# Kernel tuning notes

Hardware: AMD Instinct MI355X
Metric: run time of the kernel (lower is better)

## Reference

```python
import jax, jax.numpy as jnp
import numpy as np

SMALL = 1e-16
N = 8192      # num_nodes
D_IN = 512    # input_dim
D_LAT = 128   # latent_dim


def setup_inputs() -> dict:
    key = jax.random.key(0)
    ks = jax.random.split(key, 6)
    z = jax.random.normal(ks[0], (N, D_IN), jnp.float32)
    gamma = jax.random.uniform(ks[1], (N, D_IN), jnp.float32)
    delta = jax.random.uniform(ks[2], (N, D_IN), jnp.float32)
    lim = float(np.sqrt(6.0 / (D_IN + D_LAT)))  # glorot-uniform init
    Wz = jax.random.uniform(ks[3], (D_IN, D_LAT), jnp.float32, -lim, lim)
    Wg = jax.random.uniform(ks[4], (D_IN, D_LAT), jnp.float32, -lim, lim)
    Wd = jax.random.uniform(ks[5], (D_IN, D_LAT), jnp.float32, -lim, lim)
    return {
        "z": z, "gamma": gamma, "delta": delta,
        "Wz": Wz, "Wg": Wg, "Wd": Wd,
        "bias": jnp.float32(1.0),
        "w_gam": jnp.float32(0.5),
        "w_del": jnp.float32(0.5),
    }


def reference(z, gamma, delta, Wz, Wg, Wd, bias, w_gam, w_del):
    # column-stochastic transforms (softmax over input_dim axis, as in __init__)
    Tz = jax.nn.softmax(Wz, axis=0)
    Tg = jax.nn.softmax(Wg, axis=0)
    Td = jax.nn.softmax(Wd, axis=0)

    zd = z @ Tz                 # [N, D_LAT]
    gd_raw = gamma @ Tg         # [N, D_LAT]
    dd_raw = delta @ Td         # [N, D_LAT]
    gd = gd_raw + SMALL
    dd = dd_raw + SMALL

    z2 = zd * zd
    # dist_gam[i,j] = sum_k (zd[i,k]-zd[j,k])^2 / gd[i,k]  (sender-scaled)
    # expanded: sum_k z2_i/g_i  +  (1/g_i) . z2_j  -  2 (z_i/g_i) . z_j
    a = jnp.sum(z2 / gd, axis=1)                                  # [N]
    dist_gam = a[:, None] + (1.0 / gd) @ z2.T - 2.0 * (zd / gd) @ zd.T  # [N,N]

    # dist_del[i,j] = sum_k (zd[i,k]-zd[j,k])^2 / dd[j,k]  (receiver-scaled)
    b = jnp.sum(z2 / dd, axis=1)                                  # [N]
    dist_del = z2 @ (1.0 / dd).T - 2.0 * zd @ (zd / dd).T + b[None, :]  # [N,N]

    n = jnp.float32(N)
    x = bias - w_gam * (n * dist_gam) - w_del * (n * dist_del)
    out = jax.nn.sigmoid(x.reshape(-1))                           # [N*N]
    return out, zd, gd_raw, dd_raw
```

## Files before the change

### kernel.cpp

```cpp
#include <hip/hip_runtime.h>
#include <hip/hip_bf16.h>
#include <math.h>


#define NSZ 8192
#define DLAT 128

typedef _Float16 half8 __attribute__((ext_vector_type(8)));
typedef float f32x4 __attribute__((ext_vector_type(4)));

__device__ __forceinline__ void gl_lds16(const void* g, void* l) {
    __builtin_amdgcn_global_load_lds(
        (const __attribute__((address_space(1))) void*)g,
        (__attribute__((address_space(3))) void*)l, 16, 0, 0);
}

__device__ __forceinline__ float fast_sigmoid(float x) {
    float e = __builtin_amdgcn_exp2f(-1.44269504f * x);
    return __builtin_amdgcn_rcpf(1.0f + e);
}

__global__ void softmax_cols(const float* __restrict__ Wz, const float* __restrict__ Wg,
                             const float* __restrict__ Wd, float* __restrict__ T) {
    int col = blockIdx.x & 127;
    int m = blockIdx.x >> 7;
    const float* W = (m == 0) ? Wz : (m == 1 ? Wg : Wd);
    float* To = T + (size_t)m * 65536;
    int l = threadIdx.x;
    float v[8];
    float mx = -3.4e38f;
    for (int i = 0; i < 8; ++i) {
        v[i] = W[(size_t)(i * 64 + l) * 128 + col];
        mx = fmaxf(mx, v[i]);
    }
    for (int off = 32; off; off >>= 1) mx = fmaxf(mx, __shfl_xor(mx, off));
    float s = 0.f;
    for (int i = 0; i < 8; ++i) { v[i] = expf(v[i] - mx); s += v[i]; }
    for (int off = 32; off; off >>= 1) s += __shfl_xor(s, off);
    float inv = 1.0f / s;
    for (int i = 0; i < 8; ++i) To[(size_t)(i * 64 + l) * 128 + col] = v[i] * inv;
}

__global__ __launch_bounds__(128) void gemm3(const float* __restrict__ z,
                                             const float* __restrict__ gamma,
                                             const float* __restrict__ delta,
                                             const float* __restrict__ T,
                                             float* __restrict__ outTail) {
    int m = blockIdx.y;
    const float* A = (m == 0) ? z : (m == 1 ? gamma : delta);
    const float* B = T + (size_t)m * 65536;
    float* C = outTail + (size_t)m * (NSZ * DLAT);
    int rowBase = blockIdx.x * 32;
    __shared__ float As[32 * 34];
    int t = threadIdx.x;
    int tc = t & 15, tr = t >> 4;
    float acc[4][8] = {};
    for (int kt = 0; kt < 16; ++kt) {
        int k0 = kt * 32;
        for (int i = 0; i < 2; ++i) {
            int id = i * 128 + t;
            int r = id >> 3, kk = (id & 7) * 4;
            float4 va = *(const float4*)(A + (size_t)(rowBase + r) * 512 + k0 + kk);
            As[(kk + 0) * 34 + r] = va.x; As[(kk + 1) * 34 + r] = va.y;
            As[(kk + 2) * 34 + r] = va.z; As[(kk + 3) * 34 + r] = va.w;
        }
        __syncthreads();
        for (int kk = 0; kk < 32; ++kk) {
            float a0[4], b0[8];
            *(float4*)a0 = *(const float4*)(&As[kk * 34 + tr * 4]);
            const float* Brow = B + (size_t)(k0 + kk) * 128;
            *(float4*)b0 = *(const float4*)(Brow + tc * 4);
            *(float4*)(b0 + 4) = *(const float4*)(Brow + 64 + tc * 4);
            for (int r = 0; r < 4; ++r)
                for (int c = 0; c < 8; ++c) acc[r][c] = fmaf(a0[r], b0[c], acc[r][c]);
        }
        __syncthreads();
    }
    for (int r = 0; r < 4; ++r) {
        int row = rowBase + tr * 4 + r;
        *(float4*)(C + (size_t)row * 128 + tc * 4) = *(float4*)(&acc[r][0]);
        *(float4*)(C + (size_t)row * 128 + 64 + tc * 4) = *(float4*)(&acc[r][4]);
    }
}

__global__ void build_stacks(const float* __restrict__ zd, const float* __restrict__ gdr,
                             const float* __restrict__ ddr, _Float16* __restrict__ Afp,
                             _Float16* __restrict__ Bfp, float* __restrict__ cvec,
                             float* __restrict__ bco, const float* __restrict__ pb,
                             const float* __restrict__ pwg, const float* __restrict__ pwd) {
    int i = blockIdx.x;
    int k = threadIdx.x;
    float zv = zd[(size_t)i * 128 + k];
    float g = gdr[(size_t)i * 128 + k] + 1e-16f;
    float d = ddr[(size_t)i * 128 + k] + 1e-16f;
    float z2 = zv * zv;
    float u = 1.0f / g, p = 1.0f / d;
    float v = zv * u, q = zv * p;
    float wg = *pwg, wd = *pwd, bias = *pb;
    _Float16* Ar = Afp + (size_t)i * 512;
    _Float16* Br = Bfp + (size_t)i * 512;
    Ar[k]       = (_Float16)(wg * u);
    Ar[128 + k] = (_Float16)(wg * v);
    Ar[256 + k] = (_Float16)(wd * z2);
    Ar[384 + k] = (_Float16)(wd * zv);
    Br[k]       = (_Float16)(z2);
    Br[128 + k] = (_Float16)(-2.0f * zv);
    Br[256 + k] = (_Float16)(p);
    Br[384 + k] = (_Float16)(-2.0f * q);
    float a = z2 * u, b = z2 * p;
    for (int off = 32; off; off >>= 1) { a += __shfl_down(a, off); b += __shfl_down(b, off); }
    __shared__ float sa[2], sb[2];
    if ((k & 63) == 0) { sa[k >> 6] = a; sb[k >> 6] = b; }
    __syncthreads();
    if (k == 0) {
        cvec[i] = bias - 8192.0f * wg * (sa[0] + sa[1]);
        bco[i] = 8192.0f * wd * (sb[0] + sb[1]);
    }
}

__global__ __launch_bounds__(256) void pair_kernel(const _Float16* __restrict__ Afp,
                                                   const _Float16* __restrict__ Bfp,
                                                   const float* __restrict__ cvec,
                                                   const float* __restrict__ bco,
                                                   const float* __restrict__ pbias,
                                                   float* __restrict__ out) {
    int bid = blockIdx.x;
    int super = bid >> 6, within = bid & 63;
    int sy = super >> 3, sx = super & 7;
    int by = sy * 8 + (within >> 3), bx = sx * 8 + (within & 7);
    int iBase = by * 128, jBase = bx * 128;

    __shared__ _Float16 As[128 * 64];
    __shared__ _Float16 Bs[128 * 64];
    int t = threadIdx.x;
    int l = t & 63, w = t >> 6;
    int wm = (w >> 1) * 64, wn = (w & 1) * 64;
    int lc = l & 15, lq = l >> 4;
    f32x4 acc[4][4] = {};

    int srow = l >> 3;
    int sq = (l & 7) ^ srow;

    for (int kt = 0; kt < 8; ++kt) {
        int k0 = kt * 64;
        for (int s = 0; s < 4; ++s) {
            int rr = (w * 4 + s) * 8 + srow;
            const _Float16* ga = Afp + (size_t)(iBase + rr) * 512 + k0 + sq * 8;
            const _Float16* gb = Bfp + (size_t)(jBase + rr) * 512 + k0 + sq * 8;
            gl_lds16(ga, &As[(w * 4 + s) * 512]);
            gl_lds16(gb, &Bs[(w * 4 + s) * 512]);
        }
        __syncthreads();
        for (int ks = 0; ks < 2; ++ks) {
            half8 af[4], bf[4];
            for (int mi = 0; mi < 4; ++mi) {
                int r = wm + mi * 16 + lc;
                int q = ks * 4 + lq;
                af[mi] = *(const half8*)(&As[((r << 3) + (q ^ (r & 7))) << 3]);
            }
            for (int ni = 0; ni < 4; ++ni) {
                int r = wn + ni * 16 + lc;
                int q = ks * 4 + lq;
                bf[ni] = *(const half8*)(&Bs[((r << 3) + (q ^ (r & 7))) << 3]);
            }
            for (int mi = 0; mi < 4; ++mi)
                for (int ni = 0; ni < 4; ++ni)
                    acc[mi][ni] = __builtin_amdgcn_mfma_f32_16x16x32_f16(af[mi], bf[ni],
                                                                         acc[mi][ni], 0, 0, 0);
        }
        __syncthreads();
    }

    float bias = *pbias;
    float civ[4][4], bjv[4];
    for (int mi = 0; mi < 4; ++mi)
        for (int r = 0; r < 4; ++r)
            civ[mi][r] = cvec[iBase + wm + mi * 16 + lq * 4 + r];
    for (int ni = 0; ni < 4; ++ni) bjv[ni] = bco[jBase + wn + ni * 16 + lc];

    for (int mi = 0; mi < 4; ++mi) {
        for (int ni = 0; ni < 4; ++ni) {
            for (int r = 0; r < 4; ++r) {
                int i = iBase + wm + mi * 16 + lq * 4 + r;
                int j = jBase + wn + ni * 16 + lc;
                float x = civ[mi][r] - bjv[ni] - 8192.0f * acc[mi][ni][r];
                if (i == j) x = bias;
                out[(size_t)i * NSZ + j] = fast_sigmoid(x);
            }
        }
    }
}

extern "C" void kernel_launch(void* const* d_in, const int* in_sizes, int n_in,
                              void* d_out, int out_size, void* d_ws, size_t ws_size,
                              hipStream_t stream) {
    const float* z = (const float*)d_in[0];
    const float* gamma = (const float*)d_in[1];
    const float* delta = (const float*)d_in[2];
    const float* Wz = (const float*)d_in[3];
    const float* Wg = (const float*)d_in[4];
    const float* Wd = (const float*)d_in[5];
    const float* pb = (const float*)d_in[6];
    const float* pwg = (const float*)d_in[7];
    const float* pwd = (const float*)d_in[8];

    float* out = (float*)d_out;
    float* zd_out = out + (size_t)NSZ * NSZ;
    float* gd_out = zd_out + (size_t)NSZ * DLAT;
    float* dd_out = gd_out + (size_t)NSZ * DLAT;

    float* wsf = (float*)d_ws;
    float* T = wsf;
    float* cvec = wsf + 196608;
    float* bco = cvec + 8192;
    _Float16* Afp = (_Float16*)(bco + 8192);
    _Float16* Bfp = Afp + (size_t)NSZ * 512;

    softmax_cols<<<384, 64, 0, stream>>>(Wz, Wg, Wd, T);
    gemm3<<<dim3(256, 3), 128, 0, stream>>>(z, gamma, delta, T, zd_out);
    build_stacks<<<NSZ, 128, 0, stream>>>(zd_out, gd_out, dd_out, Afp, Bfp, cvec, bco,
                                          pb, pwg, pwd);
    pair_kernel<<<4096, 256, 0, stream>>>(Afp, Bfp, cvec, bco, pb, out);
}
```

Before: 479.7 us.

## Convert projection GEMM to fp16 MFMA with transposed fp16 softmax weights

The softmax kernel now writes the column-stochastic transforms as transposed fp16 matrices. The three input projections run on 16x16x32 fp16 MFMA instructions instead of scalar fp32 FMAs. Each block stages its whole 32x512 A tile in LDS as fp16. This is meant to cut the cost of the projection GEMM, at the price of lower precision in the zd/gd/dd outputs and a larger LDS footprint per block.

After: 428.2 us. 1.12x faster.

```diff
diff --git a/kernel.cpp b/kernel.cpp
--- a/kernel.cpp
+++ b/kernel.cpp
@@ -21,11 +21,11 @@
 }
 
 __global__ void softmax_cols(const float* __restrict__ Wz, const float* __restrict__ Wg,
-                             const float* __restrict__ Wd, float* __restrict__ T) {
+                             const float* __restrict__ Wd, _Float16* __restrict__ Tt) {
     int col = blockIdx.x & 127;
     int m = blockIdx.x >> 7;
     const float* W = (m == 0) ? Wz : (m == 1 ? Wg : Wd);
-    float* To = T + (size_t)m * 65536;
+    _Float16* To = Tt + (size_t)m * 65536 + (size_t)col * 512;
     int l = threadIdx.x;
     float v[8];
     float mx = -3.4e38f;
@@ -38,48 +38,50 @@
     for (int i = 0; i < 8; ++i) { v[i] = expf(v[i] - mx); s += v[i]; }
     for (int off = 32; off; off >>= 1) s += __shfl_xor(s, off);
     float inv = 1.0f / s;
-    for (int i = 0; i < 8; ++i) To[(size_t)(i * 64 + l) * 128 + col] = v[i] * inv;
-}
-
-__global__ __launch_bounds__(128) void gemm3(const float* __restrict__ z,
-                                             const float* __restrict__ gamma,
-                                             const float* __restrict__ delta,
-                                             const float* __restrict__ T,
-                                             float* __restrict__ outTail) {
+    for (int i = 0; i < 8; ++i) To[i * 64 + l] = (_Float16)(v[i] * inv);
+}
+
+__global__ __launch_bounds__(128) void gemm3_mfma(const float* __restrict__ z,
+                                                  const float* __restrict__ gamma,
+                                                  const float* __restrict__ delta,
+                                                  const _Float16* __restrict__ Tt,
+                                                  float* __restrict__ outTail) {
     int m = blockIdx.y;
     const float* A = (m == 0) ? z : (m == 1 ? gamma : delta);
-    const float* B = T + (size_t)m * 65536;
+    const _Float16* B = Tt + (size_t)m * 65536;
     float* C = outTail + (size_t)m * (NSZ * DLAT);
     int rowBase = blockIdx.x * 32;
-    __shared__ float As[32 * 34];
+    __shared__ _Float16 As[32 * 520];
     int t = threadIdx.x;
-    int tc = t & 15, tr = t >> 4;
-    float acc[4][8] = {};
+    for (int s = 0; s < 16; ++s) {
+        int id = s * 128 + t;
+        int row = id >> 6, c8 = id & 63;
+        const float4* src = (const float4*)(A + (size_t)(rowBase + row) * 512 + c8 * 8);
+        float4 f0 = src[0], f1 = src[1];
+        half8 h = {(_Float16)f0.x, (_Float16)f0.y, (_Float16)f0.z, (_Float16)f0.w,
+                   (_Float16)f1.x, (_Float16)f1.y, (_Float16)f1.z, (_Float16)f1.w};
+        *(half8*)(&As[row * 520 + c8 * 8]) = h;
+    }
+    __syncthreads();
+
+    int l = t & 63, w = t >> 6;
+    int lc = l & 15, lq = l >> 4;
+    int m0 = w * 16;
+    f32x4 acc[8] = {};
     for (int kt = 0; kt < 16; ++kt) {
         int k0 = kt * 32;
-        for (int i = 0; i < 2; ++i) {
-            int id = i * 128 + t;
-            int r = id >> 3, kk = (id & 7) * 4;
-            float4 va = *(const float4*)(A + (size_t)(rowBase + r) * 512 + k0 + kk);
-            As[(kk + 0) * 34 + r] = va.x; As[(kk + 1) * 34 + r] = va.y;
-            As[(kk + 2) * 34 + r] = va.z; As[(kk + 3) * 34 + r] = va.w;
-        }
-        __syncthreads();
-        for (int kk = 0; kk < 32; ++kk) {
-            float a0[4], b0[8];
-            *(float4*)a0 = *(const float4*)(&As[kk * 34 + tr * 4]);
-            const float* Brow = B + (size_t)(k0 + kk) * 128;
-            *(float4*)b0 = *(const float4*)(Brow + tc * 4);
-            *(float4*)(b0 + 4) = *(const float4*)(Brow + 64 + tc * 4);
-            for (int r = 0; r < 4; ++r)
-                for (int c = 0; c < 8; ++c) acc[r][c] = fmaf(a0[r], b0[c], acc[r][c]);
-        }
-        __syncthreads();
-    }
-    for (int r = 0; r < 4; ++r) {
-        int row = rowBase + tr * 4 + r;
-        *(float4*)(C + (size_t)row * 128 + tc * 4) = *(float4*)(&acc[r][0]);
-        *(float4*)(C + (size_t)row * 128 + 64 + tc * 4) = *(float4*)(&acc[r][4]);
+        half8 af = *(const half8*)(&As[(m0 + lc) * 520 + k0 + lq * 8]);
+        for (int ni = 0; ni < 8; ++ni) {
+            half8 bf = *(const half8*)(B + (size_t)(ni * 16 + lc) * 512 + k0 + lq * 8);
+            acc[ni] = __builtin_amdgcn_mfma_f32_16x16x32_f16(af, bf, acc[ni], 0, 0, 0);
+        }
+    }
+    for (int ni = 0; ni < 8; ++ni) {
+        for (int r = 0; r < 4; ++r) {
+            int row = rowBase + m0 + lq * 4 + r;
+            int col = ni * 16 + lc;
+            C[(size_t)row * 128 + col] = acc[ni][r];
+        }
     }
 }
 
@@ -210,14 +212,14 @@
     float* dd_out = gd_out + (size_t)NSZ * DLAT;
 
     float* wsf = (float*)d_ws;
-    float* T = wsf;
-    float* cvec = wsf + 196608;
+    _Float16* Tt = (_Float16*)wsf;
+    float* cvec = wsf + 98304;
     float* bco = cvec + 8192;
     _Float16* Afp = (_Float16*)(bco + 8192);
     _Float16* Bfp = Afp + (size_t)NSZ * 512;
 
-    softmax_cols<<<384, 64, 0, stream>>>(Wz, Wg, Wd, T);
-    gemm3<<<dim3(256, 3), 128, 0, stream>>>(z, gamma, delta, T, zd_out);
+    softmax_cols<<<384, 64, 0, stream>>>(Wz, Wg, Wd, Tt);
+    gemm3_mfma<<<dim3(256, 3), 128, 0, stream>>>(z, gamma, delta, Tt, zd_out);
     build_stacks<<<NSZ, 128, 0, stream>>>(zd_out, gd_out, dd_out, Afp, Bfp, cvec, bco,
                                           pb, pwg, pwd);
     pair_kernel<<<4096, 256, 0, stream>>>(Afp, Bfp, cvec, bco, pb, out);
```
